# Kernel optimization log

Measured on AMD Instinct MI355X. Metric: run time of the kernel, lower is better.

The kernel has to match this reference:

```python
import jax, jax.numpy as jnp
import numpy as np

N = 50000      # nodes
E = 400000     # edges (before self-loops)
D_IN = 128     # input node features
H1, C1 = 8, 64   # layer-1 heads / per-head channels (concat -> 512)
H2, C2 = 1, 16   # layer-2 heads / per-head channels (mean -> 16)
NEG_SLOPE = 0.2  # PyG GATConv default leaky-relu slope


def setup_inputs() -> dict:
    key = jax.random.key(0)
    ks = jax.random.split(key, 10)
    x = jax.random.normal(ks[0], (N, D_IN), jnp.float32)
    edge_index = jax.random.randint(ks[1], (2, E), 0, N, dtype=jnp.int32)
    s1 = D_IN ** -0.5
    s2 = (H1 * C1) ** -0.5
    return {
        "x": x,
        "edge_index": edge_index,
        "W1": jax.random.normal(ks[2], (D_IN, H1 * C1), jnp.float32) * s1,
        "a1_src": jax.random.normal(ks[3], (H1, C1), jnp.float32) * (C1 ** -0.5),
        "a1_dst": jax.random.normal(ks[4], (H1, C1), jnp.float32) * (C1 ** -0.5),
        "b1": jnp.zeros((H1 * C1,), jnp.float32),
        "W2": jax.random.normal(ks[5], (H1 * C1, H2 * C2), jnp.float32) * s2,
        "a2_src": jax.random.normal(ks[6], (H2, C2), jnp.float32) * (C2 ** -0.5),
        "a2_dst": jax.random.normal(ks[7], (H2, C2), jnp.float32) * (C2 ** -0.5),
        "b2": jnp.zeros((C2,), jnp.float32),
    }


def gat_layer(x, W, a_src, a_dst, bias, src, dst, H, C, concat):
    n = x.shape[0]
    h = (x @ W).reshape(n, H, C)                       # [N,H,C]
    # per-node attention halves (PyG: alpha = a_src . h_src + a_dst . h_dst)
    al_src = jnp.einsum('nhc,hc->nh', h, a_src)        # [N,H]
    al_dst = jnp.einsum('nhc,hc->nh', h, a_dst)
    logits = jax.nn.leaky_relu(al_src[src] + al_dst[dst], NEG_SLOPE)  # [E,H]
    # segment softmax over incoming edges of each destination node
    m = jax.ops.segment_max(logits, dst, num_segments=n)
    e = jnp.exp(logits - m[dst])
    denom = jax.ops.segment_sum(e, dst, num_segments=n)
    alpha = e / denom[dst]                             # [E,H]
    out = jax.ops.segment_sum(alpha[:, :, None] * h[src], dst, num_segments=n)  # [N,H,C]
    out = out.reshape(n, H * C) if concat else out.mean(axis=1)
    return out + bias


def reference(x, edge_index, W1, a1_src, a1_dst, b1, W2, a2_src, a2_dst, b2):
    n = x.shape[0]
    # PyG GATConv adds self-loops by default (applied in each layer)
    loops = jnp.arange(n, dtype=edge_index.dtype)
    src = jnp.concatenate([edge_index[0], loops])
    dst = jnp.concatenate([edge_index[1], loops])
    h1 = gat_layer(x, W1, a1_src, a1_dst, b1, src, dst, H1, C1, True)   # [N,512]
    h1 = jax.nn.elu(h1)
    return gat_layer(h1, W2, a2_src, a2_dst, b2, src, dst, H2, C2, False)  # [N,16]
```

## Files before the change

kernel.cpp:

```cpp
#include <hip/hip_runtime.h>
#include <math.h>

#define N_NODES 50000
#define N_EDGES 400000
#define N_TOT   450000
#define NEG 0.2f
#define CAP 64

typedef __attribute__((ext_vector_type(8))) short bf16x8;
typedef __attribute__((ext_vector_type(4))) float f32x4;

__device__ __forceinline__ float lrelu(float x) { return x > 0.f ? x : NEG * x; }

__device__ __forceinline__ unsigned short f2bf(float f) {
    unsigned u = __float_as_uint(f);
    unsigned r = u + 0x7FFFu + ((u >> 16) & 1u);
    return (unsigned short)(r >> 16);
}
__device__ __forceinline__ float bf2f(unsigned short h) {
    return __uint_as_float(((unsigned)h) << 16);
}

__global__ void k_init(const float* __restrict__ W1, unsigned short* W1hiT,
                       const float* __restrict__ W2, unsigned short* W2hiT,
                       const float* __restrict__ a1s, const float* __restrict__ a1d,
                       unsigned short* W1aThi, unsigned short* W1aTlo,
                       int* cursor) {
    int i = blockIdx.x * 256 + threadIdx.x;
    if (i < 128 * 512) {
        int col = i & 511, k = i >> 9;
        W1hiT[col * 128 + k] = f2bf(W1[k * 512 + col]);
    } else if (i < 128 * 512 + 512 * 16) {
        int j = i - 128 * 512;
        int col = j & 15, k = j >> 4;
        W2hiT[col * 512 + k] = f2bf(W2[k * 16 + col]);
    } else if (i < 128 * 512 + 512 * 16 + 128 * 16) {
        int j = i - (128 * 512 + 512 * 16);
        int c16 = j & 15, k = j >> 4;
        int hd = c16 & 7;
        const float* av = (c16 < 8) ? a1s : a1d;
        float acc = 0.f;
#pragma unroll 8
        for (int c = 0; c < 64; c++)
            acc = fmaf(W1[k * 512 + hd * 64 + c], av[hd * 64 + c], acc);
        unsigned short h = f2bf(acc);
        W1aThi[c16 * 128 + k] = h;
        W1aTlo[c16 * 128 + k] = f2bf(acc - bf2f(h));
    } else {
        int j = i - (128 * 512 + 512 * 16 + 128 * 16);
        if (j < N_NODES) cursor[j] = 0;
    }
}

#define SCAT 256
__global__ __launch_bounds__(256) void k_sg1(const int* __restrict__ ei,
                                             int* __restrict__ cursor,
                                             int* __restrict__ colsrc,
                                             const float* __restrict__ x,
                                             const unsigned short* __restrict__ W1hiT,
                                             const unsigned short* __restrict__ W1aThi,
                                             const unsigned short* __restrict__ W1aTlo,
                                             unsigned short* __restrict__ h1b,
                                             float* __restrict__ al1s,
                                             float* __restrict__ al1d) {
    __shared__ unsigned short xs_hi[64 * 136];
    if (blockIdx.x < SCAT) {
        int gtid = blockIdx.x * 256 + threadIdx.x;
        for (int i = gtid; i < N_TOT; i += SCAT * 256) {
            int src, dst;
            if (i < N_EDGES) { src = ei[i]; dst = ei[N_EDGES + i]; }
            else             { src = dst = i - N_EDGES; }
            int pos = atomicAdd(&cursor[dst], 1);
            if (pos < CAP) colsrc[dst * CAP + pos] = src;
        }
        return;
    }
    const int t = threadIdx.x;
    const int rb = (blockIdx.x - SCAT) * 64;

#pragma unroll
    for (int i = 0; i < 8; i++) {
        int idx = t + 256 * i;
        int r = idx >> 5;
        int k = (idx & 31) * 4;
        int gr = rb + r;
        float4 v = make_float4(0.f, 0.f, 0.f, 0.f);
        if (gr < N_NODES) v = *reinterpret_cast<const float4*>(&x[gr * 128 + k]);
        ushort4 hi;
        hi.x = f2bf(v.x); hi.y = f2bf(v.y); hi.z = f2bf(v.z); hi.w = f2bf(v.w);
        *reinterpret_cast<ushort4*>(&xs_hi[r * 136 + k]) = hi;
    }
    __syncthreads();

    const int lane = t & 63;
    const int w = t >> 6;
    const int kbase = (lane >> 4) * 8;
    const int colloc = (w << 4) + (lane & 15);

#pragma unroll
    for (int pr = 0; pr < 4; pr++) {
        bf16x8 bhi[2][4];
#pragma unroll
        for (int si = 0; si < 2; si++) {
            int col = (pr * 2 + si) * 64 + colloc;
#pragma unroll
            for (int kc = 0; kc < 4; kc++)
                bhi[si][kc] = *reinterpret_cast<const bf16x8*>(&W1hiT[col * 128 + kc * 32 + kbase]);
        }
#pragma unroll
        for (int mt = 0; mt < 4; mt++) {
            const int arow = mt * 16 + (lane & 15);
            bf16x8 ah[4];
#pragma unroll
            for (int kc = 0; kc < 4; kc++)
                ah[kc] = *reinterpret_cast<const bf16x8*>(&xs_hi[arow * 136 + kc * 32 + kbase]);
#pragma unroll
            for (int si = 0; si < 2; si++) {
                f32x4 acc = {0.f, 0.f, 0.f, 0.f};
#pragma unroll
                for (int kc = 0; kc < 4; kc++)
                    acc = __builtin_amdgcn_mfma_f32_16x16x32_bf16(ah[kc], bhi[si][kc], acc, 0, 0, 0);
                const int col = (pr * 2 + si) * 64 + colloc;
                const int r0 = rb + mt * 16 + (lane >> 4) * 4;
#pragma unroll
                for (int r = 0; r < 4; r++) {
                    int row = r0 + r;
                    if (row < N_NODES) h1b[row * 512 + col] = f2bf(acc[r]);
                }
            }
        }
    }

    {
        const int c16 = lane & 15;
        bf16x8 bh[4], bl[4];
#pragma unroll
        for (int kc = 0; kc < 4; kc++) {
            bh[kc] = *reinterpret_cast<const bf16x8*>(&W1aThi[c16 * 128 + kc * 32 + kbase]);
            bl[kc] = *reinterpret_cast<const bf16x8*>(&W1aTlo[c16 * 128 + kc * 32 + kbase]);
        }
        const int arow = (w << 4) + (lane & 15);
        f32x4 acc = {0.f, 0.f, 0.f, 0.f};
#pragma unroll
        for (int kc = 0; kc < 4; kc++) {
            bf16x8 ah = *reinterpret_cast<const bf16x8*>(&xs_hi[arow * 136 + kc * 32 + kbase]);
            acc = __builtin_amdgcn_mfma_f32_16x16x32_bf16(ah, bh[kc], acc, 0, 0, 0);
            acc = __builtin_amdgcn_mfma_f32_16x16x32_bf16(ah, bl[kc], acc, 0, 0, 0);
        }
        const int r0 = rb + (w << 4) + (lane >> 4) * 4;
#pragma unroll
        for (int r = 0; r < 4; r++) {
            int row = r0 + r;
            if (row < N_NODES) {
                if (c16 < 8) al1s[row * 8 + c16] = acc[r];
                else         al1d[row * 8 + (c16 - 8)] = acc[r];
            }
        }
    }
}

__global__ __launch_bounds__(256) void k_agg1(const int* __restrict__ cursor,
                                              const int* __restrict__ colsrc,
                                              const float* __restrict__ al1s,
                                              const float* __restrict__ al1d,
                                              const unsigned short* __restrict__ h1b,
                                              const float* __restrict__ b1,
                                              unsigned short* __restrict__ h1a) {
    __shared__ float pw[4][8 * 65];
    int wid = threadIdx.x >> 6;
    int lane = threadIdx.x & 63;
    int n = blockIdx.x * 4 + wid;
    if (n >= N_NODES) return;
    int cnt = min(cursor[n], CAP);
    const int eb = n * CAP;
    const float4 d0 = *reinterpret_cast<const float4*>(&al1d[n * 8]);
    const float4 d1 = *reinterpret_cast<const float4*>(&al1d[n * 8 + 4]);
    int hA = lane >> 4, hB = hA + 4;
    int cA = 4 * lane, cB = 256 + 4 * lane;
    f32x4 aA = {0.f, 0.f, 0.f, 0.f}, aB = {0.f, 0.f, 0.f, 0.f};
    float sA = 0.f, sB = 0.f;
    float* mypw = pw[wid];

    int s0 = 0;
    float p[8];
    if (lane < cnt) {
        s0 = colsrc[eb + lane];
        const float4 u0 = *reinterpret_cast<const float4*>(&al1s[s0 * 8]);
        const float4 u1 = *reinterpret_cast<const float4*>(&al1s[s0 * 8 + 4]);
        p[0] = __expf(fminf(lrelu(u0.x + d0.x), 60.f));
        p[1] = __expf(fminf(lrelu(u0.y + d0.y), 60.f));
        p[2] = __expf(fminf(lrelu(u0.z + d0.z), 60.f));
        p[3] = __expf(fminf(lrelu(u0.w + d0.w), 60.f));
        p[4] = __expf(fminf(lrelu(u1.x + d1.x), 60.f));
        p[5] = __expf(fminf(lrelu(u1.y + d1.y), 60.f));
        p[6] = __expf(fminf(lrelu(u1.z + d1.z), 60.f));
        p[7] = __expf(fminf(lrelu(u1.w + d1.w), 60.f));
    } else {
#pragma unroll
        for (int h = 0; h < 8; h++) p[h] = 0.f;
    }
#pragma unroll
    for (int h = 0; h < 8; h++) mypw[h * 65 + lane] = p[h];

    for (int j = 0; j < cnt; j++) {
        int s = __shfl(s0, j, 64);
        float wA = mypw[hA * 65 + j];
        float wB = mypw[hB * 65 + j];
        ushort4 hvA = *reinterpret_cast<const ushort4*>(&h1b[s * 512 + cA]);
        ushort4 hvB = *reinterpret_cast<const ushort4*>(&h1b[s * 512 + cB]);
        sA += wA; sB += wB;
        aA[0] = fmaf(wA, bf2f(hvA.x), aA[0]);
        aA[1] = fmaf(wA, bf2f(hvA.y), aA[1]);
        aA[2] = fmaf(wA, bf2f(hvA.z), aA[2]);
        aA[3] = fmaf(wA, bf2f(hvA.w), aA[3]);
        aB[0] = fmaf(wB, bf2f(hvB.x), aB[0]);
        aB[1] = fmaf(wB, bf2f(hvB.y), aB[1]);
        aB[2] = fmaf(wB, bf2f(hvB.z), aB[2]);
        aB[3] = fmaf(wB, bf2f(hvB.w), aB[3]);
    }
    float iA = 1.f / sA, iB = 1.f / sB;
    const float4 bA = *reinterpret_cast<const float4*>(&b1[cA]);
    const float4 bB = *reinterpret_cast<const float4*>(&b1[cB]);
    float vA[4], vB[4];
    vA[0] = aA[0] * iA + bA.x; vA[1] = aA[1] * iA + bA.y;
    vA[2] = aA[2] * iA + bA.z; vA[3] = aA[3] * iA + bA.w;
    vB[0] = aB[0] * iB + bB.x; vB[1] = aB[1] * iB + bB.y;
    vB[2] = aB[2] * iB + bB.z; vB[3] = aB[3] * iB + bB.w;
#pragma unroll
    for (int k = 0; k < 4; k++) {
        vA[k] = vA[k] > 0.f ? vA[k] : __expf(vA[k]) - 1.f;
        vB[k] = vB[k] > 0.f ? vB[k] : __expf(vB[k]) - 1.f;
    }
    ushort4 oA, oB;
    oA.x = f2bf(vA[0]); oA.y = f2bf(vA[1]); oA.z = f2bf(vA[2]); oA.w = f2bf(vA[3]);
    oB.x = f2bf(vB[0]); oB.y = f2bf(vB[1]); oB.z = f2bf(vB[2]); oB.w = f2bf(vB[3]);
    *reinterpret_cast<ushort4*>(&h1a[n * 512 + cA]) = oA;
    *reinterpret_cast<ushort4*>(&h1a[n * 512 + cB]) = oB;
}

__global__ __launch_bounds__(256) void k_gemm2(const unsigned short* __restrict__ h1a,
                                               const unsigned short* __restrict__ W2hiT,
                                               const float* __restrict__ a2s,
                                               const float* __restrict__ a2d,
                                               unsigned short* __restrict__ h2b,
                                               float* __restrict__ al2s,
                                               float* __restrict__ al2d) {
    __shared__ unsigned short as_hi[64 * 520];
    const int t = threadIdx.x;
    const int rb = blockIdx.x * 64;

#pragma unroll
    for (int i = 0; i < 16; i++) {
        int idx = t + 256 * i;
        int r = idx >> 6;
        int k8 = (idx & 63) * 8;
        int gr = rb + r;
        uint4 v = make_uint4(0, 0, 0, 0);
        if (gr < N_NODES) v = *reinterpret_cast<const uint4*>(&h1a[gr * 512 + k8]);
        *reinterpret_cast<uint4*>(&as_hi[r * 520 + k8]) = v;
    }
    __syncthreads();

    const int lane = t & 63;
    const int w = t >> 6;
    const int col = lane & 15;
    const int kbase = (lane >> 4) * 8;
    const int arow = (w << 4) + (lane & 15);

    f32x4 acc = {0.f, 0.f, 0.f, 0.f};
#pragma unroll
    for (int kc = 0; kc < 16; kc++) {
        bf16x8 bh = *reinterpret_cast<const bf16x8*>(&W2hiT[col * 512 + kc * 32 + kbase]);
        bf16x8 ah = *reinterpret_cast<const bf16x8*>(&as_hi[arow * 520 + kc * 32 + kbase]);
        acc = __builtin_amdgcn_mfma_f32_16x16x32_bf16(ah, bh, acc, 0, 0, 0);
    }
    const float as_c = a2s[col];
    const float ad_c = a2d[col];
    const int rloc = (w << 4) + (lane >> 4) * 4;
#pragma unroll
    for (int r = 0; r < 4; r++) {
        int row = rb + rloc + r;
        float ps = acc[r] * as_c;
        float pd = acc[r] * ad_c;
        ps += __shfl_xor(ps, 1, 64); pd += __shfl_xor(pd, 1, 64);
        ps += __shfl_xor(ps, 2, 64); pd += __shfl_xor(pd, 2, 64);
        ps += __shfl_xor(ps, 4, 64); pd += __shfl_xor(pd, 4, 64);
        ps += __shfl_xor(ps, 8, 64); pd += __shfl_xor(pd, 8, 64);
        if (row < N_NODES) {
            h2b[row * 16 + col] = f2bf(acc[r]);
            if ((lane & 15) == 0) { al2s[row] = ps; al2d[row] = pd; }
        }
    }
}

__global__ __launch_bounds__(256) void k_agg2(const int* __restrict__ cursor,
                                              const int* __restrict__ colsrc,
                                              const float* __restrict__ al2s,
                                              const float* __restrict__ al2d,
                                              const unsigned short* __restrict__ h2b,
                                              const float* __restrict__ b2,
                                              float* __restrict__ out) {
    int wv = threadIdx.x >> 6, lane = threadIdx.x & 63;
    int n = blockIdx.x * 4 + wv;
    if (n >= N_NODES) return;
    int cnt = min(cursor[n], CAP);
    const int eb = n * CAP;
    float ald = al2d[n];
    int c = lane & 15, q = lane >> 4;
    float acc = 0.f, smL = 0.f;
    int e = q;
    for (; e + 4 < cnt; e += 8) {
        int s0 = colsrc[eb + e];
        int s1 = colsrc[eb + e + 4];
        float w0 = __expf(fminf(lrelu(al2s[s0] + ald), 60.f));
        float w1 = __expf(fminf(lrelu(al2s[s1] + ald), 60.f));
        unsigned short v0 = h2b[s0 * 16 + c];
        unsigned short v1 = h2b[s1 * 16 + c];
        smL += w0 + w1;
        acc = fmaf(w0, bf2f(v0), acc);
        acc = fmaf(w1, bf2f(v1), acc);
    }
    for (; e < cnt; e += 4) {
        int s = colsrc[eb + e];
        float w = __expf(fminf(lrelu(al2s[s] + ald), 60.f));
        smL += w;
        acc = fmaf(w, bf2f(h2b[s * 16 + c]), acc);
    }
    acc += __shfl_xor(acc, 16, 64); smL += __shfl_xor(smL, 16, 64);
    acc += __shfl_xor(acc, 32, 64); smL += __shfl_xor(smL, 32, 64);
    if (q == 0) out[n * 16 + c] = acc / smL + b2[c];
}

extern "C" void kernel_launch(void* const* d_in, const int* in_sizes, int n_in,
                              void* d_out, int out_size, void* d_ws, size_t ws_size,
                              hipStream_t stream) {
    const float* x   = (const float*)d_in[0];
    const int*   ei  = (const int*)d_in[1];
    const float* W1  = (const float*)d_in[2];
    const float* a1s = (const float*)d_in[3];
    const float* a1d = (const float*)d_in[4];
    const float* b1  = (const float*)d_in[5];
    const float* W2  = (const float*)d_in[6];
    const float* a2s = (const float*)d_in[7];
    const float* a2d = (const float*)d_in[8];
    const float* b2  = (const float*)d_in[9];
    float* out = (float*)d_out;

    char* ws = (char*)d_ws;
    unsigned short* h1b = (unsigned short*)(ws + 0);
    unsigned short* h1a = (unsigned short*)(ws + 51200000);
    unsigned short* h2b = (unsigned short*)(ws + 102400000);
    float* al1s = (float*)(ws + 105600000);
    float* al1d = (float*)(ws + 107200000);
    float* al2s = (float*)(ws + 108800000);
    float* al2d = (float*)(ws + 109000000);
    int* cursor = (int*)(ws + 109200000);
    int* colsrc = (int*)(ws + 109400000);
    unsigned short* W1hiT  = (unsigned short*)(ws + 122200000);
    unsigned short* W2hiT  = (unsigned short*)(ws + 122336000);
    unsigned short* W1aThi = (unsigned short*)(ws + 122352384);
    unsigned short* W1aTlo = (unsigned short*)(ws + 122356480);

    k_init<<<492, 256, 0, stream>>>(W1, W1hiT, W2, W2hiT, a1s, a1d, W1aThi, W1aTlo, cursor);

    k_sg1<<<SCAT + (N_NODES + 63) / 64, 256, 0, stream>>>(ei, cursor, colsrc, x,
                                                          W1hiT, W1aThi, W1aTlo,
                                                          h1b, al1s, al1d);

    k_agg1<<<(N_NODES + 3) / 4, 256, 0, stream>>>(cursor, colsrc, al1s, al1d, h1b, b1, h1a);

    k_gemm2<<<(N_NODES + 63) / 64, 256, 0, stream>>>(h1a, W2hiT, a2s, a2d, h2b, al2s, al2d);
    k_agg2<<<(N_NODES + 3) / 4, 256, 0, stream>>>(cursor, colsrc, al2s, al2d, h2b, b2, out);
}
```

Baseline: 242.1 us.

## Fuse layer-2 projection and attention logits into layer-1 aggregation kernel

Removes the separate k_gemm2 kernel and the 512-wide bf16 h1a intermediate. After computing the ELU output, each wave multiplies its 512 values by W2 in registers and reduces the 16 outputs with a butterfly of shuffles, then writes h2b and the layer-2 attention logits. This avoids writing and re-reading about 51 MB of intermediate data and one launch. In exchange it adds 16x6 cross-lane shuffles and scalar FMAs per node in place of MFMA, plus extra register pressure in the aggregation kernel.

```diff
diff --git a/kernel.cpp b/kernel.cpp
--- a/kernel.cpp
+++ b/kernel.cpp
@@ -165,7 +165,12 @@
                                               const float* __restrict__ al1d,
                                               const unsigned short* __restrict__ h1b,
                                               const float* __restrict__ b1,
-                                              unsigned short* __restrict__ h1a) {
+                                              const unsigned short* __restrict__ W2hiT,
+                                              const float* __restrict__ a2s,
+                                              const float* __restrict__ a2d,
+                                              unsigned short* __restrict__ h2b,
+                                              float* __restrict__ al2s,
+                                              float* __restrict__ al2d) {
     __shared__ float pw[4][8 * 65];
     int wid = threadIdx.x >> 6;
     int lane = threadIdx.x & 63;
@@ -231,65 +236,35 @@
         vA[k] = vA[k] > 0.f ? vA[k] : __expf(vA[k]) - 1.f;
         vB[k] = vB[k] > 0.f ? vB[k] : __expf(vB[k]) - 1.f;
     }
-    ushort4 oA, oB;
-    oA.x = f2bf(vA[0]); oA.y = f2bf(vA[1]); oA.z = f2bf(vA[2]); oA.w = f2bf(vA[3]);
-    oB.x = f2bf(vB[0]); oB.y = f2bf(vB[1]); oB.z = f2bf(vB[2]); oB.w = f2bf(vB[3]);
-    *reinterpret_cast<ushort4*>(&h1a[n * 512 + cA]) = oA;
-    *reinterpret_cast<ushort4*>(&h1a[n * 512 + cB]) = oB;
-}
-
-__global__ __launch_bounds__(256) void k_gemm2(const unsigned short* __restrict__ h1a,
-                                               const unsigned short* __restrict__ W2hiT,
-                                               const float* __restrict__ a2s,
-                                               const float* __restrict__ a2d,
-                                               unsigned short* __restrict__ h2b,
-                                               float* __restrict__ al2s,
-                                               float* __restrict__ al2d) {
-    __shared__ unsigned short as_hi[64 * 520];
-    const int t = threadIdx.x;
-    const int rb = blockIdx.x * 64;
-
-#pragma unroll
-    for (int i = 0; i < 16; i++) {
-        int idx = t + 256 * i;
-        int r = idx >> 6;
-        int k8 = (idx & 63) * 8;
-        int gr = rb + r;
-        uint4 v = make_uint4(0, 0, 0, 0);
-        if (gr < N_NODES) v = *reinterpret_cast<const uint4*>(&h1a[gr * 512 + k8]);
-        *reinterpret_cast<uint4*>(&as_hi[r * 520 + k8]) = v;
-    }
-    __syncthreads();
-
-    const int lane = t & 63;
-    const int w = t >> 6;
-    const int col = lane & 15;
-    const int kbase = (lane >> 4) * 8;
-    const int arow = (w << 4) + (lane & 15);
-
-    f32x4 acc = {0.f, 0.f, 0.f, 0.f};
-#pragma unroll
-    for (int kc = 0; kc < 16; kc++) {
-        bf16x8 bh = *reinterpret_cast<const bf16x8*>(&W2hiT[col * 512 + kc * 32 + kbase]);
-        bf16x8 ah = *reinterpret_cast<const bf16x8*>(&as_hi[arow * 520 + kc * 32 + kbase]);
-        acc = __builtin_amdgcn_mfma_f32_16x16x32_bf16(ah, bh, acc, 0, 0, 0);
-    }
-    const float as_c = a2s[col];
-    const float ad_c = a2d[col];
-    const int rloc = (w << 4) + (lane >> 4) * 4;
-#pragma unroll
-    for (int r = 0; r < 4; r++) {
-        int row = rb + rloc + r;
-        float ps = acc[r] * as_c;
-        float pd = acc[r] * ad_c;
-        ps += __shfl_xor(ps, 1, 64); pd += __shfl_xor(pd, 1, 64);
-        ps += __shfl_xor(ps, 2, 64); pd += __shfl_xor(pd, 2, 64);
-        ps += __shfl_xor(ps, 4, 64); pd += __shfl_xor(pd, 4, 64);
-        ps += __shfl_xor(ps, 8, 64); pd += __shfl_xor(pd, 8, 64);
-        if (row < N_NODES) {
-            h2b[row * 16 + col] = f2bf(acc[r]);
-            if ((lane & 15) == 0) { al2s[row] = ps; al2d[row] = pd; }
-        }
+
+    float p2[16];
+#pragma unroll
+    for (int c = 0; c < 16; c++) {
+        ushort4 wA = *reinterpret_cast<const ushort4*>(&W2hiT[c * 512 + cA]);
+        ushort4 wB = *reinterpret_cast<const ushort4*>(&W2hiT[c * 512 + cB]);
+        float s2 = vA[0] * bf2f(wA.x) + vA[1] * bf2f(wA.y)
+                 + vA[2] * bf2f(wA.z) + vA[3] * bf2f(wA.w)
+                 + vB[0] * bf2f(wB.x) + vB[1] * bf2f(wB.y)
+                 + vB[2] * bf2f(wB.z) + vB[3] * bf2f(wB.w);
+        p2[c] = s2;
+    }
+#pragma unroll
+    for (int off = 1; off < 64; off <<= 1) {
+#pragma unroll
+        for (int c = 0; c < 16; c++) p2[c] += __shfl_xor(p2[c], off, 64);
+    }
+    float ps = 0.f, pd = 0.f;
+#pragma unroll
+    for (int c = 0; c < 16; c++) {
+        ps = fmaf(p2[c], a2s[c], ps);
+        pd = fmaf(p2[c], a2d[c], pd);
+    }
+    if (lane == 0) { al2s[n] = ps; al2d[n] = pd; }
+    if (lane < 16) {
+        float hv = p2[0];
+#pragma unroll
+        for (int c = 1; c < 16; c++) hv = (lane == c) ? p2[c] : hv;
+        h2b[n * 16 + lane] = f2bf(hv);
     }
 }
 
@@ -348,18 +323,17 @@
 
     char* ws = (char*)d_ws;
     unsigned short* h1b = (unsigned short*)(ws + 0);
-    unsigned short* h1a = (unsigned short*)(ws + 51200000);
-    unsigned short* h2b = (unsigned short*)(ws + 102400000);
-    float* al1s = (float*)(ws + 105600000);
-    float* al1d = (float*)(ws + 107200000);
-    float* al2s = (float*)(ws + 108800000);
-    float* al2d = (float*)(ws + 109000000);
-    int* cursor = (int*)(ws + 109200000);
-    int* colsrc = (int*)(ws + 109400000);
-    unsigned short* W1hiT  = (unsigned short*)(ws + 122200000);
-    unsigned short* W2hiT  = (unsigned short*)(ws + 122336000);
-    unsigned short* W1aThi = (unsigned short*)(ws + 122352384);
-    unsigned short* W1aTlo = (unsigned short*)(ws + 122356480);
+    unsigned short* h2b = (unsigned short*)(ws + 51200000);
+    float* al1s = (float*)(ws + 54400000);
+    float* al1d = (float*)(ws + 56000000);
+    float* al2s = (float*)(ws + 57600000);
+    float* al2d = (float*)(ws + 57800000);
+    int* cursor = (int*)(ws + 58000000);
+    int* colsrc = (int*)(ws + 58200000);
+    unsigned short* W1hiT  = (unsigned short*)(ws + 71000000);
+    unsigned short* W2hiT  = (unsigned short*)(ws + 71136000);
+    unsigned short* W1aThi = (unsigned short*)(ws + 71152384);
+    unsigned short* W1aTlo = (unsigned short*)(ws + 71156480);
 
     k_init<<<492, 256, 0, stream>>>(W1, W1hiT, W2, W2hiT, a1s, a1d, W1aThi, W1aTlo, cursor);
 
@@ -367,8 +341,8 @@
                                                           W1hiT, W1aThi, W1aTlo,
                                                           h1b, al1s, al1d);
 
-    k_agg1<<<(N_NODES + 3) / 4, 256, 0, stream>>>(cursor, colsrc, al1s, al1d, h1b, b1, h1a);
-
-    k_gemm2<<<(N_NODES + 63) / 64, 256, 0, stream>>>(h1a, W2hiT, a2s, a2d, h2b, al2s, al2d);
+    k_agg1<<<(N_NODES + 3) / 4, 256, 0, stream>>>(cursor, colsrc, al1s, al1d, h1b, b1,
+                                                  W2hiT, a2s, a2d, h2b, al2s, al2d);
+
     k_agg2<<<(N_NODES + 3) / 4, 256, 0, stream>>>(cursor, colsrc, al2s, al2d, h2b, b2, out);
 }
```

New measurement: 244.3 us. Within noise of the previous version (+0.9%).
